# Kernel tuning notes

Measured on AMD Instinct MI355X. Metric: run time of the kernel, lower is better.

The kernel has to match this reference:

```python
import jax, jax.numpy as jnp
import numpy as np

N_NODES = 50000
N_EDGES = 800000
D_FEAT = 128
EMBED = 128
HEADS = 8
HEAD_DIM = EMBED // HEADS


def setup_inputs() -> dict:
    key = jax.random.key(0)
    ks = jax.random.split(key, 10)
    xavier = jax.nn.initializers.xavier_normal()
    return {
        "nodes": jax.random.normal(ks[0], (N_NODES, D_FEAT), jnp.float32),
        "edges": jax.random.normal(ks[1], (N_EDGES, D_FEAT), jnp.float32),
        "senders": jax.random.randint(ks[2], (N_EDGES,), 0, N_NODES, jnp.int32),
        "receivers": jax.random.randint(ks[3], (N_EDGES,), 0, N_NODES, jnp.int32),
        "Ws_k": xavier(ks[4], (D_FEAT, EMBED), jnp.float32),
        "Ws_b": jnp.zeros((EMBED,), jnp.float32),
        "Wr_k": xavier(ks[5], (D_FEAT, EMBED), jnp.float32),
        "Wr_b": jnp.zeros((EMBED,), jnp.float32),
        "We_k": xavier(ks[6], (D_FEAT, EMBED), jnp.float32),
        "We_b": jnp.zeros((EMBED,), jnp.float32),
        "a": xavier(ks[7], (HEADS, HEAD_DIM), jnp.float32),
    }


def reference(nodes, edges, senders, receivers, Ws_k, Ws_b, Wr_k, Wr_b, We_k, We_b, a):
    N = nodes.shape[0]
    E = edges.shape[0]
    H, D = a.shape
    # Node-level projections (linear, so equivalent to projecting gathered edge endpoints)
    hs = nodes @ Ws_k + Ws_b            # [N, HD]  (W_s on sent attributes)
    hr = nodes @ Wr_k + Wr_b            # [N, HD]  (W_r on received attributes)
    he = edges @ We_k + We_b            # [E, HD]  (W_e on edge attributes)
    sent = hs[senders]                  # [E, HD]
    x = jax.nn.leaky_relu(sent + hr[receivers] + he)  # default slope 0.01, as original
    xh = x.reshape(E, H, D)
    logits = jnp.sum(xh * a, axis=-1)   # [E, H]
    # segment_softmax over receivers (stable: subtract per-segment max)
    mx = jax.ops.segment_max(logits, receivers, num_segments=N)  # [N, H]
    mx = jnp.where(jnp.isfinite(mx), mx, 0.0)
    ex = jnp.exp(logits - mx[receivers])                         # [E, H]
    denom = jax.ops.segment_sum(ex, receivers, num_segments=N)   # [N, H]
    w = ex / denom[receivers]                                    # [E, H]
    msg = (w[..., None] * sent.reshape(E, H, D)).reshape(E, H * D)
    out = jax.ops.segment_sum(msg, receivers, num_segments=N)    # [N, HD]
    return out
```

## Files before the change

### kernel.cpp

```cpp
#include <hip/hip_runtime.h>

#define N_NODES 50000
#define N_EDGES 800000
#define D 128
#define HEADS 8

typedef __attribute__((ext_vector_type(8))) short short8b;
typedef __attribute__((ext_vector_type(4))) float f32x4;

__device__ __forceinline__ unsigned short f2bf_rne(float f) {
    unsigned int u = __float_as_uint(f);
    u += 0x7FFFu + ((u >> 16) & 1u);
    return (unsigned short)(u >> 16);
}
__device__ __forceinline__ float bf2f(unsigned short u) {
    return __uint_as_float(((unsigned int)u) << 16);
}

#define K1_ROWS 256
__global__ __launch_bounds__(256, 3) void k_node_proj_mfma(
    const float* __restrict__ nodes,
    const float* __restrict__ Ws, const float* __restrict__ bs,
    const float* __restrict__ Wr, const float* __restrict__ br,
    unsigned short* __restrict__ hsb, unsigned short* __restrict__ hrb)
{
    __shared__ __align__(16) unsigned short WT[D][136];
    __shared__ __align__(16) unsigned short At[64][136];
    const int ntiles = (N_NODES + K1_ROWS - 1) / K1_ROWS;
    int bx = blockIdx.x;
    int proj = (bx >= ntiles) ? 1 : 0;
    int tile = proj ? (bx - ntiles) : bx;
    const float* W    = proj ? Wr : Ws;
    const float* bias = proj ? br : bs;
    unsigned short* outp = proj ? hrb : hsb;
    int t = threadIdx.x;
    int lane = t & 63;
    int wv = t >> 6;
    int lg = lane >> 4;
    int li = lane & 15;

    #pragma unroll 8
    for (int j = 0; j < 64; ++j) {
        int idx = t + 256 * j;
        int k = idx >> 7, c = idx & 127;
        WT[c][k] = f2bf_rne(W[idx]);
    }
    float b_ct[8];
    #pragma unroll
    for (int ct = 0; ct < 8; ++ct) b_ct[ct] = bias[ct * 16 + li];

    #pragma unroll 1
    for (int sub = 0; sub < 4; ++sub) {
        int row0 = tile * K1_ROWS + sub * 64;
        if (row0 >= N_NODES) break;
        __syncthreads();
        {
            const float4* Nv = (const float4*)nodes;
            #pragma unroll
            for (int j = 0; j < 8; ++j) {
                int fi = t + 256 * j;
                int r = row0 + (fi >> 5);
                float4 v = make_float4(0.f, 0.f, 0.f, 0.f);
                if (r < N_NODES) v = Nv[(size_t)r * 32 + (fi & 31)];
                ushort4 b;
                b.x = f2bf_rne(v.x); b.y = f2bf_rne(v.y);
                b.z = f2bf_rne(v.z); b.w = f2bf_rne(v.w);
                *(ushort4*)&At[fi >> 5][(fi & 31) * 4] = b;
            }
        }
        __syncthreads();

        short8b afr[4];
        #pragma unroll
        for (int kb = 0; kb < 4; ++kb)
            afr[kb] = *(const short8b*)&At[wv * 16 + li][kb * 32 + lg * 8];

        #pragma unroll
        for (int ct = 0; ct < 8; ++ct) {
            f32x4 acc = {0.f, 0.f, 0.f, 0.f};
            #pragma unroll
            for (int kb = 0; kb < 4; ++kb) {
                short8b bfr = *(const short8b*)&WT[ct * 16 + li][kb * 32 + lg * 8];
                acc = __builtin_amdgcn_mfma_f32_16x16x32_bf16(afr[kb], bfr, acc, 0, 0, 0);
            }
            #pragma unroll
            for (int j = 0; j < 4; ++j) {
                int r = row0 + wv * 16 + lg * 4 + j;
                if (r < N_NODES)
                    outp[(size_t)r * D + ct * 16 + li] = f2bf_rne(acc[j] + b_ct[ct]);
            }
        }
    }
}

__global__ __launch_bounds__(256) void k_hist(
    const int* __restrict__ receivers, int* __restrict__ deg)
{
    int i = blockIdx.x * 256 + threadIdx.x;
    if (i < N_EDGES) atomicAdd(&deg[receivers[i]], 1);
}

#define SCAN_CHUNK 49
__global__ __launch_bounds__(1024) void k_scan(
    const int* __restrict__ deg, int* __restrict__ rowptr, int* __restrict__ cursor)
{
    __shared__ int sm[1024];
    int t = threadIdx.x;
    int base = t * SCAN_CHUNK;
    int lsum = 0;
    #pragma unroll 4
    for (int i = 0; i < SCAN_CHUNK; ++i) {
        int idx = base + i;
        if (idx < N_NODES) lsum += deg[idx];
    }
    sm[t] = lsum;
    __syncthreads();
    for (int off = 1; off < 1024; off <<= 1) {
        int v = (t >= off) ? sm[t - off] : 0;
        __syncthreads();
        sm[t] += v;
        __syncthreads();
    }
    int run = (t > 0) ? sm[t - 1] : 0;
    for (int i = 0; i < SCAN_CHUNK; ++i) {
        int idx = base + i;
        if (idx < N_NODES) {
            rowptr[idx] = run;
            cursor[idx] = run;
            run += deg[idx];
        }
    }
    if (t == 1023) rowptr[N_NODES] = sm[1023];
}

__global__ __launch_bounds__(256) void k_fill(
    const int* __restrict__ receivers, const int* __restrict__ senders,
    int* __restrict__ cursor,
    int* __restrict__ eids, int* __restrict__ s_csr, int* __restrict__ r_csr)
{
    int i = blockIdx.x * 256 + threadIdx.x;
    if (i < N_EDGES) {
        int r = receivers[i];
        int pos = atomicAdd(&cursor[r], 1);
        eids[pos]  = i;
        s_csr[pos] = senders[i];
        r_csr[pos] = r;
    }
}

#define BLK_E 64
__global__ __launch_bounds__(256, 3) void k_edge_logits_mfma(
    const float* __restrict__ edges,
    const int* __restrict__ eids, const int* __restrict__ s_csr,
    const int* __restrict__ r_csr,
    const float* __restrict__ We, const float* __restrict__ be,
    const float* __restrict__ a,
    const unsigned short* __restrict__ hsb, const unsigned short* __restrict__ hrb,
    float* __restrict__ ex)
{
    __shared__ __align__(16) unsigned short WeT[D][136];
    __shared__ __align__(16) unsigned short Et[BLK_E][136];
    int t = threadIdx.x;
    int lane = t & 63;
    int wv = t >> 6;
    int lg = lane >> 4;
    int li = lane & 15;

    #pragma unroll 8
    for (int j = 0; j < 64; ++j) {
        int idx = t + 256 * j;
        int k = idx >> 7, c = idx & 127;
        WeT[c][k] = f2bf_rne(We[idx]);
    }
    float a_h[HEADS], be_h[HEADS];
    #pragma unroll
    for (int h = 0; h < HEADS; ++h) {
        a_h[h]  = a[h * 16 + li];
        be_h[h] = be[h * 16 + li];
    }
    int jm = li & 3;

    const int ntiles = N_EDGES / BLK_E;
    for (int tile = blockIdx.x; tile < ntiles; tile += gridDim.x) {
        int p0 = tile * BLK_E;

        int sj[4], rj[4];
        #pragma unroll
        for (int j = 0; j < 4; ++j) {
            int pos = p0 + wv * 16 + lg * 4 + j;
            sj[j] = s_csr[pos];
            rj[j] = r_csr[pos];
        }

        __syncthreads();
        {
            const float4* Ev = (const float4*)edges;
            #pragma unroll
            for (int j = 0; j < 8; ++j) {
                int fi = t + 256 * j;
                int e = eids[p0 + (fi >> 5)];
                float4 v = Ev[(size_t)e * 32 + (fi & 31)];
                ushort4 b;
                b.x = f2bf_rne(v.x); b.y = f2bf_rne(v.y);
                b.z = f2bf_rne(v.z); b.w = f2bf_rne(v.w);
                *(ushort4*)&Et[fi >> 5][(fi & 31) * 4] = b;
            }
        }

        unsigned short g_hs[4][HEADS], g_hr[4][HEADS];
        #pragma unroll
        for (int j = 0; j < 4; ++j) {
            const unsigned short* hsrow = hsb + (size_t)sj[j] * D + li;
            const unsigned short* hrrow = hrb + (size_t)rj[j] * D + li;
            #pragma unroll
            for (int h = 0; h < HEADS; ++h) {
                g_hs[j][h] = hsrow[h * 16];
                g_hr[j][h] = hrrow[h * 16];
            }
        }

        __syncthreads();

        short8b afr[4];
        int erow = wv * 16 + li;
        #pragma unroll
        for (int kb = 0; kb < 4; ++kb)
            afr[kb] = *(const short8b*)&Et[erow][kb * 32 + lg * 8];

        #pragma unroll
        for (int h = 0; h < HEADS; ++h) {
            f32x4 acc = {0.f, 0.f, 0.f, 0.f};
            #pragma unroll
            for (int kb = 0; kb < 4; ++kb) {
                short8b bfr = *(const short8b*)&WeT[h * 16 + li][kb * 32 + lg * 8];
                acc = __builtin_amdgcn_mfma_f32_16x16x32_bf16(afr[kb], bfr, acc, 0, 0, 0);
            }
            float p[4];
            #pragma unroll
            for (int j = 0; j < 4; ++j) {
                float x = acc[j] + be_h[h] + bf2f(g_hs[j][h]) + bf2f(g_hr[j][h]);
                x = x > 0.f ? x : 0.01f * x;
                p[j] = x * a_h[h];
            }
            #pragma unroll
            for (int j = 0; j < 4; ++j) {
                p[j] += __shfl_xor(p[j], 1);
                p[j] += __shfl_xor(p[j], 2);
            }
            float q = (jm & 1) ? ((jm & 2) ? p[3] : p[1])
                               : ((jm & 2) ? p[2] : p[0]);
            q += __shfl_xor(q, 4);
            q += __shfl_xor(q, 8);
            float e_ = __expf(q);
            if (li < 4) {
                int pos = p0 + wv * 16 + lg * 4 + li;
                ex[(size_t)pos * HEADS + h] = e_;
            }
        }
    }
}

__global__ __launch_bounds__(256) void k_gather_out(
    const int* __restrict__ rowptr, const int* __restrict__ s_csr,
    const unsigned short* __restrict__ hsb, const float* __restrict__ ex,
    float* __restrict__ out)
{
    int r = blockIdx.x * 4 + (threadIdx.x >> 6);
    int l = threadIdx.x & 63;
    int h = l >> 3;
    int beg = rowptr[r], end = rowptr[r + 1];

    float2 acc = make_float2(0.f, 0.f);
    float dsum = 0.f;
    for (int j0 = beg; j0 < end; j0 += 8) {
        int cnt = end - j0;
        int s[8]; float w[8];
        #pragma unroll
        for (int q = 0; q < 8; ++q)
            if (q < cnt) { s[q] = s_csr[j0 + q]; w[q] = ex[(size_t)(j0 + q) * HEADS + h]; }
        #pragma unroll
        for (int q = 0; q < 8; ++q)
            if (q < cnt) {
                ushort2 hv = *(const ushort2*)&hsb[(size_t)s[q] * D + 2 * l];
                acc.x += w[q] * bf2f(hv.x);
                acc.y += w[q] * bf2f(hv.y);
                dsum  += w[q];
            }
    }
    float inv = (end > beg && dsum != 0.f) ? (1.0f / dsum) : 0.f;
    acc.x *= inv; acc.y *= inv;
    *(float2*)&out[(size_t)r * D + 2 * l] = acc;
}

extern "C" void kernel_launch(void* const* d_in, const int* in_sizes, int n_in,
                              void* d_out, int out_size, void* d_ws, size_t ws_size,
                              hipStream_t stream) {
    const float* nodes     = (const float*)d_in[0];
    const float* edges     = (const float*)d_in[1];
    const int*   senders   = (const int*)d_in[2];
    const int*   receivers = (const int*)d_in[3];
    const float* Ws = (const float*)d_in[4];
    const float* bs = (const float*)d_in[5];
    const float* Wr = (const float*)d_in[6];
    const float* br = (const float*)d_in[7];
    const float* We = (const float*)d_in[8];
    const float* be = (const float*)d_in[9];
    const float* a  = (const float*)d_in[10];
    float* out = (float*)d_out;

    unsigned short* hsb = (unsigned short*)d_ws;
    unsigned short* hrb = hsb + (size_t)N_NODES * D;
    float* ex   = (float*)(hrb + (size_t)N_NODES * D);
    int* deg    = (int*)(ex + (size_t)N_EDGES * HEADS);
    int* rowptr = deg + N_NODES;
    int* cursor = rowptr + N_NODES + 1;
    int* eids   = cursor + N_NODES;
    int* s_csr  = eids + N_EDGES;
    int* r_csr  = s_csr + N_EDGES;

    hipMemsetAsync(deg, 0, N_NODES * sizeof(int), stream);
    k_hist<<<N_EDGES / 256, 256, 0, stream>>>(receivers, deg);
    k_scan<<<1, 1024, 0, stream>>>(deg, rowptr, cursor);
    k_fill<<<N_EDGES / 256, 256, 0, stream>>>(receivers, senders, cursor,
                                              eids, s_csr, r_csr);
    int ntiles_n = (N_NODES + K1_ROWS - 1) / K1_ROWS;
    k_node_proj_mfma<<<ntiles_n * 2, 256, 0, stream>>>(nodes, Ws, bs, Wr, br, hsb, hrb);
    k_edge_logits_mfma<<<2048, 256, 0, stream>>>(edges, eids, s_csr, r_csr,
                                                 We, be, a, hsb, hrb, ex);
    k_gather_out<<<N_NODES / 4, 256, 0, stream>>>(rowptr, s_csr, hsb, ex, out);
}
```

Baseline: 463.2 us.

## Load edge features straight into MFMA registers, drop LDS staging and barriers

The edge-logit kernel now has each lane load its own edge row slice from global memory and convert it to bf16 directly into the MFMA A-fragment registers. This removes the shared-memory staging tile and both per-tile block barriers. The grid shrinks to 768 persistent blocks, and the gather kernel batches 16 neighbours per iteration instead of 8 to raise memory-level parallelism. In exchange, register pressure goes up and each lane's global loads are less coalesced (32-byte chunks per lane).

```diff
diff --git a/kernel.cpp b/kernel.cpp
--- a/kernel.cpp
+++ b/kernel.cpp
@@ -159,7 +159,6 @@
     float* __restrict__ ex)
 {
     __shared__ __align__(16) unsigned short WeT[D][136];
-    __shared__ __align__(16) unsigned short Et[BLK_E][136];
     int t = threadIdx.x;
     int lane = t & 63;
     int wv = t >> 6;
@@ -179,34 +178,29 @@
         be_h[h] = be[h * 16 + li];
     }
     int jm = li & 3;
+    __syncthreads();
 
     const int ntiles = N_EDGES / BLK_E;
     for (int tile = blockIdx.x; tile < ntiles; tile += gridDim.x) {
-        int p0 = tile * BLK_E;
-
+        int pbase = tile * BLK_E + wv * 16;
+
+        int erow = eids[pbase + li];
         int sj[4], rj[4];
         #pragma unroll
         for (int j = 0; j < 4; ++j) {
-            int pos = p0 + wv * 16 + lg * 4 + j;
-            sj[j] = s_csr[pos];
-            rj[j] = r_csr[pos];
-        }
-
-        __syncthreads();
+            sj[j] = s_csr[pbase + lg * 4 + j];
+            rj[j] = r_csr[pbase + lg * 4 + j];
+        }
+
+        float4 ea[4][2];
         {
-            const float4* Ev = (const float4*)edges;
-            #pragma unroll
-            for (int j = 0; j < 8; ++j) {
-                int fi = t + 256 * j;
-                int e = eids[p0 + (fi >> 5)];
-                float4 v = Ev[(size_t)e * 32 + (fi & 31)];
-                ushort4 b;
-                b.x = f2bf_rne(v.x); b.y = f2bf_rne(v.y);
-                b.z = f2bf_rne(v.z); b.w = f2bf_rne(v.w);
-                *(ushort4*)&Et[fi >> 5][(fi & 31) * 4] = b;
-            }
-        }
-
+            const float* erp = edges + (size_t)erow * D + lg * 8;
+            #pragma unroll
+            for (int kb = 0; kb < 4; ++kb) {
+                ea[kb][0] = *(const float4*)(erp + kb * 32);
+                ea[kb][1] = *(const float4*)(erp + kb * 32 + 4);
+            }
+        }
         unsigned short g_hs[4][HEADS], g_hr[4][HEADS];
         #pragma unroll
         for (int j = 0; j < 4; ++j) {
@@ -219,13 +213,18 @@
             }
         }
 
-        __syncthreads();
-
         short8b afr[4];
-        int erow = wv * 16 + li;
-        #pragma unroll
-        for (int kb = 0; kb < 4; ++kb)
-            afr[kb] = *(const short8b*)&Et[erow][kb * 32 + lg * 8];
+        #pragma unroll
+        for (int kb = 0; kb < 4; ++kb) {
+            afr[kb][0] = (short)f2bf_rne(ea[kb][0].x);
+            afr[kb][1] = (short)f2bf_rne(ea[kb][0].y);
+            afr[kb][2] = (short)f2bf_rne(ea[kb][0].z);
+            afr[kb][3] = (short)f2bf_rne(ea[kb][0].w);
+            afr[kb][4] = (short)f2bf_rne(ea[kb][1].x);
+            afr[kb][5] = (short)f2bf_rne(ea[kb][1].y);
+            afr[kb][6] = (short)f2bf_rne(ea[kb][1].z);
+            afr[kb][7] = (short)f2bf_rne(ea[kb][1].w);
+        }
 
         #pragma unroll
         for (int h = 0; h < HEADS; ++h) {
@@ -253,7 +252,7 @@
             q += __shfl_xor(q, 8);
             float e_ = __expf(q);
             if (li < 4) {
-                int pos = p0 + wv * 16 + lg * 4 + li;
+                int pos = pbase + lg * 4 + li;
                 ex[(size_t)pos * HEADS + h] = e_;
             }
         }
@@ -272,14 +271,14 @@
 
     float2 acc = make_float2(0.f, 0.f);
     float dsum = 0.f;
-    for (int j0 = beg; j0 < end; j0 += 8) {
+    for (int j0 = beg; j0 < end; j0 += 16) {
         int cnt = end - j0;
-        int s[8]; float w[8];
-        #pragma unroll
-        for (int q = 0; q < 8; ++q)
+        int s[16]; float w[16];
+        #pragma unroll
+        for (int q = 0; q < 16; ++q)
             if (q < cnt) { s[q] = s_csr[j0 + q]; w[q] = ex[(size_t)(j0 + q) * HEADS + h]; }
         #pragma unroll
-        for (int q = 0; q < 8; ++q)
+        for (int q = 0; q < 16; ++q)
             if (q < cnt) {
                 ushort2 hv = *(const ushort2*)&hsb[(size_t)s[q] * D + 2 * l];
                 acc.x += w[q] * bf2f(hv.x);
@@ -325,7 +324,7 @@
                                               eids, s_csr, r_csr);
     int ntiles_n = (N_NODES + K1_ROWS - 1) / K1_ROWS;
     k_node_proj_mfma<<<ntiles_n * 2, 256, 0, stream>>>(nodes, Ws, bs, Wr, br, hsb, hrb);
-    k_edge_logits_mfma<<<2048, 256, 0, stream>>>(edges, eids, s_csr, r_csr,
-                                                 We, be, a, hsb, hrb, ex);
+    k_edge_logits_mfma<<<768, 256, 0, stream>>>(edges, eids, s_csr, r_csr,
+                                                We, be, a, hsb, hrb, ex);
     k_gather_out<<<N_NODES / 4, 256, 0, stream>>>(rowptr, s_csr, hsb, ex, out);
 }
```

New measurement: 635.7 us. 1.37x slower.
